# Optimization experiments

Measured on AMD Instinct MI355X. Metric: run time of the kernel, lower is better.

## Reference

```python
import jax, jax.numpy as jnp
import numpy as np


def setup_inputs() -> dict:
    key = jax.random.key(0)
    k1, k2, k3 = jax.random.split(key, 3)
    num, c_in, c_out, nx, ny, din, dout = 128, 3, 8, 31, 31, 4, 6
    x = jax.random.normal(k1, (num, c_in, din, nx + 1, ny + 1), dtype=jnp.float32)
    tensors = jax.random.normal(k2, (c_in, c_out, nx, ny, din, din, din, din, dout), dtype=jnp.float32)
    bias = jax.random.normal(k3, (c_out, nx, ny, dout), dtype=jnp.float32) * 1e-8
    return {"x": x, "tensors": tensors, "bias": bias}


def reference(x, tensors, bias):
    # x: [num, c_in, din, sx, sy]; tensors: [c_in, c_out, nx, ny, din,din,din,din, dout]
    num, c_in, din, sx, sy = x.shape
    X, Y = sx - 1, sy - 1  # == nx, ny
    c_out, dout = tensors.shape[1], tensors.shape[-1]
    # four 2x2-patch corners, each [num, c_in, din, X, Y]
    a = x[:, :, :, :-1, :-1]
    b = x[:, :, :, 1:, :-1]
    c = x[:, :, :, :-1, 1:]
    d = x[:, :, :, 1:, 1:]
    # outer product of the four corner vectors -> rank-4 local feature [num, c_in, din^4, X, Y]
    ab = jnp.einsum('ncixy,ncjxy->ncijxy', a, b)
    cd = jnp.einsum('nckxy,nclxy->ncklxy', c, d)
    patch = jnp.einsum('ncijxy,ncklxy->ncijklxy', ab, cd)
    patch = patch.reshape(num, c_in, din ** 4, X, Y)
    # per-position weight: [c_in, c_out, X, Y, din^4, dout]
    w = tensors.reshape(c_in, c_out, X, Y, din ** 4, dout)
    out = jnp.einsum('ncmxy,cpxymo->npoxy', patch, w)  # [num, c_out, dout, X, Y]
    out = out + bias.transpose(0, 3, 1, 2)[None]  # bias -> [1, c_out, dout, X, Y]
    return out
```

## Files before the change

### kernel.cpp

```cpp
#include <hip/hip_runtime.h>
#include <hip/hip_bf16.h>


typedef __attribute__((ext_vector_type(8))) short short8;
typedef __attribute__((ext_vector_type(4))) float floatx4;

#define WS_ELEMS (961u * 6144u)
#define SW_COLS 136

static __device__ __forceinline__ unsigned pkbf(float lo, float hi) {
  __hip_bfloat162 h = __float22bfloat162_rn(make_float2(lo, hi));
  union { __hip_bfloat162 h; unsigned u; } v;
  v.h = h;
  return v.u;
}

template <bool TO_WS>
__global__ __launch_bounds__(256, 4)
void ttn_conv_mfma(const float* __restrict__ x,
                   const float* __restrict__ tensors,
                   const float* __restrict__ bias,
                   float* __restrict__ dst) {
  __shared__ __align__(16) unsigned short sW[2][48 * SW_COLS];

  const int site = blockIdx.x;
  const int xx = site / 31, yy = site - xx * 31;
  const int t = threadIdx.x;
  const int lane = t & 63, wave = t >> 6;
  const int row = lane & 15, quad = lane >> 4;

  const int p_st = t >> 5, q_st = t & 31;

  floatx4 acc[2][3];
#pragma unroll
  for (int i0 = 0; i0 < 2; ++i0)
#pragma unroll
    for (int j0 = 0; j0 < 3; ++j0)
      acc[i0][j0] = (floatx4){0.f, 0.f, 0.f, 0.f};

  float a4[2][4], b2[2][2], cd8[2][8];
  float2 rAC[2][4], rBD[2][4];
  float4 wv[6];

  auto loadPair = [&](int s) {
    const int c = s >> 1;
    const float* base = tensors + ((size_t)((c * 8 + p_st) * 961 + site)) * 1536;
#pragma unroll
    for (int h = 0; h < 2; ++h) {
      const float* src = base + (size_t)((2 * (s & 1) + h) * 64 + 2 * q_st) * 6;
      wv[h * 3 + 0] = *(const float4*)src;
      wv[h * 3 + 1] = *(const float4*)(src + 4);
      wv[h * 3 + 2] = *(const float4*)(src + 8);
    }
  };
  auto storePair = [&](int buf) {
#pragma unroll
    for (int h = 0; h < 2; ++h) {
      const float4 w0 = wv[h * 3], w1 = wv[h * 3 + 1], w2 = wv[h * 3 + 2];
      const float vv[12] = {w0.x, w0.y, w0.z, w0.w, w1.x, w1.y,
                            w1.z, w1.w, w2.x, w2.y, w2.z, w2.w};
#pragma unroll
      for (int o = 0; o < 6; ++o)
        *(unsigned*)&sW[buf][(p_st * 6 + o) * SW_COLS + h * 64 + 2 * q_st] =
            pkbf(vv[o], vv[o + 6]);
    }
  };
  auto loadRaw = [&](int c) {
#pragma unroll
    for (int mt = 0; mt < 2; ++mt) {
      const int n = wave * 32 + mt * 16 + row;
      const float* xb = x + ((size_t)n * 3 + c) * 4096 + xx * 32 + yy;
#pragma unroll
      for (int i = 0; i < 4; ++i) {
        rAC[mt][i] = *(const float2*)(xb + i * 1024);
        rBD[mt][i] = *(const float2*)(xb + i * 1024 + 32);
      }
    }
  };
  auto cvtFactors = [&]() {
    const int qh = quad >> 1, ql = quad & 1;
#pragma unroll
    for (int mt = 0; mt < 2; ++mt) {
#pragma unroll
      for (int i = 0; i < 4; ++i) a4[mt][i] = rAC[mt][i].x;
      b2[mt][0] = qh ? rBD[mt][1].x : rBD[mt][0].x;
      b2[mt][1] = qh ? rBD[mt][3].x : rBD[mt][2].x;
      const float cq0 = ql ? rAC[mt][2].y : rAC[mt][0].y;
      const float cq1 = ql ? rAC[mt][3].y : rAC[mt][1].y;
#pragma unroll
      for (int j = 0; j < 8; ++j)
        cd8[mt][j] = (j < 4 ? cq0 : cq1) * rBD[mt][j & 3].y;
    }
  };

  loadPair(0);
  loadRaw(0);
  cvtFactors();
  storePair(0);
  loadPair(1);
  __syncthreads();

#pragma unroll
  for (int s = 0; s < 6; ++s) {
    const int bp = s & 1;
    if (s <= 4) storePair(1 - bp);
    if (s <= 3) loadPair(s + 2);
    if (s == 1) loadRaw(1);
    if (s == 3) loadRaw(2);
    if (s == 2 || s == 4) cvtFactors();

#pragma unroll
    for (int ks = 0; ks < 4; ++ks) {
      const int mb = 2 * (s & 1) + (ks >> 1);
      short8 bfr[3];
#pragma unroll
      for (int nt = 0; nt < 3; ++nt)
        bfr[nt] = *(const short8*)&sW[bp][(nt * 16 + row) * SW_COLS + ks * 32 + quad * 8];
#pragma unroll
      for (int mt = 0; mt < 2; ++mt) {
        const float ab = a4[mt][mb] * b2[mt][ks & 1];
        union { unsigned u[4]; short8 s8; } af;
#pragma unroll
        for (int jj = 0; jj < 4; ++jj)
          af.u[jj] = pkbf(ab * cd8[mt][2 * jj], ab * cd8[mt][2 * jj + 1]);
#pragma unroll
        for (int nt = 0; nt < 3; ++nt)
          acc[mt][nt] = __builtin_amdgcn_mfma_f32_16x16x32_bf16(
              af.s8, bfr[nt], acc[mt][nt], 0, 0, 0);
      }
    }
    if (s < 5) __syncthreads();
  }

  if (TO_WS) {
#pragma unroll
    for (int mt = 0; mt < 2; ++mt)
#pragma unroll
      for (int r = 0; r < 4; ++r) {
        const int n = wave * 32 + mt * 16 + quad * 4 + r;
#pragma unroll
        for (int nt = 0; nt < 3; ++nt) {
          const int po = nt * 16 + row;
          dst[(size_t)site * 6144 + n * 48 + po] = acc[mt][nt][r];
        }
      }
  } else {
#pragma unroll
    for (int mt = 0; mt < 2; ++mt)
#pragma unroll
      for (int r = 0; r < 4; ++r) {
        const int n = wave * 32 + mt * 16 + quad * 4 + r;
#pragma unroll
        for (int nt = 0; nt < 3; ++nt) {
          const int po = nt * 16 + row;
          const int p = po / 6, o = po - p * 6;
          dst[(size_t)(n * 48 + po) * 961 + site] =
              acc[mt][nt][r] + bias[(p * 961 + site) * 6 + o];
        }
      }
  }
}

__global__ __launch_bounds__(256, 8)
void ttn_transpose_bias(const float* __restrict__ ws,
                        const float* __restrict__ bias,
                        float* __restrict__ out) {
  __shared__ float tile[32][33];
  const int f0 = blockIdx.x * 32;
  const int s0 = blockIdx.y * 32;
  const int tx = threadIdx.x;
  const int ty = threadIdx.y;

#pragma unroll
  for (int rr = 0; rr < 4; ++rr) {
    const int srow = ty + rr * 8;
    const int site = s0 + srow;
    if (site < 961)
      tile[srow][tx] = ws[(size_t)site * 6144 + f0 + tx];
  }
  __syncthreads();

#pragma unroll
  for (int rr = 0; rr < 4; ++rr) {
    const int fy = ty + rr * 8;
    const int f = f0 + fy;
    const int site = s0 + tx;
    if (site < 961) {
      const int po = f % 48;
      const int p = po / 6, o = po - p * 6;
      out[(size_t)f * 961 + site] = tile[tx][fy] + bias[(p * 961 + site) * 6 + o];
    }
  }
}

extern "C" void kernel_launch(void* const* d_in, const int* in_sizes, int n_in,
                              void* d_out, int out_size, void* d_ws, size_t ws_size,
                              hipStream_t stream) {
  const float* x       = (const float*)d_in[0];
  const float* tensors = (const float*)d_in[1];
  const float* bias    = (const float*)d_in[2];
  float* out           = (float*)d_out;

  const size_t need = (size_t)WS_ELEMS * sizeof(float);
  if (d_ws != nullptr && ws_size >= need) {
    float* ws = (float*)d_ws;
    hipLaunchKernelGGL((ttn_conv_mfma<true>), dim3(961), dim3(256), 0, stream,
                       x, tensors, bias, ws);
    hipLaunchKernelGGL(ttn_transpose_bias, dim3(192, 31), dim3(32, 8), 0, stream,
                       ws, bias, out);
  } else {
    hipLaunchKernelGGL((ttn_conv_mfma<false>), dim3(961), dim3(256), 0, stream,
                       x, tensors, bias, out);
  }
}
```

Measured before the change: 245.4 us.

## Pre-convert weights to bf16 MFMA layout and feed GEMM from registers

Adds a separate pass that converts the fp32 per-site weights into bf16 in a layout matching the MFMA B-fragment. The GEMM kernel then loads those fragments straight from global memory into double-buffered registers. This removes the shared-memory staging, the in-loop bf16 packing and the block barriers from the main kernel. The cost is an extra kernel launch, roughly double the total weight traffic (read fp32, write bf16, read bf16 again) and a larger workspace requirement. The old fused path is kept as a fallback when the workspace is too small.

```diff
diff --git a/kernel.cpp b/kernel.cpp
--- a/kernel.cpp
+++ b/kernel.cpp
@@ -6,7 +6,8 @@
 typedef __attribute__((ext_vector_type(4))) float floatx4;
 
 #define WS_ELEMS (961u * 6144u)
-#define SW_COLS 136
+#define WP_OFFSET (32u * 1024u * 1024u)
+#define WP_BYTES ((size_t)23064u * 3072u)
 
 static __device__ __forceinline__ unsigned pkbf(float lo, float hi) {
   __hip_bfloat162 h = __float22bfloat162_rn(make_float2(lo, hi));
@@ -15,21 +16,39 @@
   return v.u;
 }
 
-template <bool TO_WS>
-__global__ __launch_bounds__(256, 4)
-void ttn_conv_mfma(const float* __restrict__ x,
-                   const float* __restrict__ tensors,
-                   const float* __restrict__ bias,
-                   float* __restrict__ dst) {
-  __shared__ __align__(16) unsigned short sW[2][48 * SW_COLS];
-
+__global__ __launch_bounds__(256)
+void ttn_wprep(const float* __restrict__ tensors, unsigned* __restrict__ wp) {
+  const int idx = blockIdx.x * 256 + threadIdx.x;
+  const int cps = idx >> 7, q = idx & 127;
+  const float* src = tensors + (size_t)cps * 1536 + q * 12;
+  const float4 v0 = *(const float4*)src;
+  const float4 v1 = *(const float4*)(src + 4);
+  const float4 v2 = *(const float4*)(src + 8);
+  const float vv[12] = {v0.x, v0.y, v0.z, v0.w, v1.x, v1.y,
+                        v1.z, v1.w, v2.x, v2.y, v2.z, v2.w};
+  unsigned* dst = wp + (size_t)cps * 768 + q;
+#pragma unroll
+  for (int o = 0; o < 6; ++o)
+    dst[o * 128] = pkbf(vv[o], vv[o + 6]);
+}
+
+__global__ __launch_bounds__(256, 3)
+void ttn_gemm(const float* __restrict__ x,
+              const unsigned short* __restrict__ wp,
+              float* __restrict__ ws) {
   const int site = blockIdx.x;
   const int xx = site / 31, yy = site - xx * 31;
-  const int t = threadIdx.x;
-  const int lane = t & 63, wave = t >> 6;
+  const int t = threadIdx.x, lane = t & 63, wave = t >> 6;
   const int row = lane & 15, quad = lane >> 4;
 
-  const int p_st = t >> 5, q_st = t & 31;
+  int baseo[3];
+#pragma unroll
+  for (int nt = 0; nt < 3; ++nt) {
+    const int po = nt * 16 + row;
+    const int p = po / 6, o = po - p * 6;
+    baseo[nt] = (p * 961 + site) * 1536 + o * 256 + quad * 8;
+  }
+  const size_t cstride = (size_t)8 * 961 * 1536;
 
   floatx4 acc[2][3];
 #pragma unroll
@@ -39,86 +58,54 @@
       acc[i0][j0] = (floatx4){0.f, 0.f, 0.f, 0.f};
 
   float a4[2][4], b2[2][2], cd8[2][8];
-  float2 rAC[2][4], rBD[2][4];
-  float4 wv[6];
-
-  auto loadPair = [&](int s) {
-    const int c = s >> 1;
-    const float* base = tensors + ((size_t)((c * 8 + p_st) * 961 + site)) * 1536;
-#pragma unroll
-    for (int h = 0; h < 2; ++h) {
-      const float* src = base + (size_t)((2 * (s & 1) + h) * 64 + 2 * q_st) * 6;
-      wv[h * 3 + 0] = *(const float4*)src;
-      wv[h * 3 + 1] = *(const float4*)(src + 4);
-      wv[h * 3 + 2] = *(const float4*)(src + 8);
-    }
-  };
-  auto storePair = [&](int buf) {
-#pragma unroll
-    for (int h = 0; h < 2; ++h) {
-      const float4 w0 = wv[h * 3], w1 = wv[h * 3 + 1], w2 = wv[h * 3 + 2];
-      const float vv[12] = {w0.x, w0.y, w0.z, w0.w, w1.x, w1.y,
-                            w1.z, w1.w, w2.x, w2.y, w2.z, w2.w};
-#pragma unroll
-      for (int o = 0; o < 6; ++o)
-        *(unsigned*)&sW[buf][(p_st * 6 + o) * SW_COLS + h * 64 + 2 * q_st] =
-            pkbf(vv[o], vv[o + 6]);
-    }
-  };
-  auto loadRaw = [&](int c) {
+  short8 wbuf[2][6];
+
+  auto loadChunk = [&](int ch, int buf) {
+    const unsigned short* base = wp + (size_t)(ch >> 2) * cstride + (ch & 3) * 64;
+#pragma unroll
+    for (int nt = 0; nt < 3; ++nt)
+#pragma unroll
+      for (int ks = 0; ks < 2; ++ks)
+        wbuf[buf][nt * 2 + ks] = *(const short8*)(base + baseo[nt] + ks * 32);
+  };
+  auto loadFactors = [&](int c) {
+    const int qh = quad >> 1, ql = quad & 1;
 #pragma unroll
     for (int mt = 0; mt < 2; ++mt) {
       const int n = wave * 32 + mt * 16 + row;
       const float* xb = x + ((size_t)n * 3 + c) * 4096 + xx * 32 + yy;
+      float2 rAC[4], rBD[4];
 #pragma unroll
       for (int i = 0; i < 4; ++i) {
-        rAC[mt][i] = *(const float2*)(xb + i * 1024);
-        rBD[mt][i] = *(const float2*)(xb + i * 1024 + 32);
-      }
-    }
-  };
-  auto cvtFactors = [&]() {
-    const int qh = quad >> 1, ql = quad & 1;
-#pragma unroll
-    for (int mt = 0; mt < 2; ++mt) {
-#pragma unroll
-      for (int i = 0; i < 4; ++i) a4[mt][i] = rAC[mt][i].x;
-      b2[mt][0] = qh ? rBD[mt][1].x : rBD[mt][0].x;
-      b2[mt][1] = qh ? rBD[mt][3].x : rBD[mt][2].x;
-      const float cq0 = ql ? rAC[mt][2].y : rAC[mt][0].y;
-      const float cq1 = ql ? rAC[mt][3].y : rAC[mt][1].y;
+        rAC[i] = *(const float2*)(xb + i * 1024);
+        rBD[i] = *(const float2*)(xb + i * 1024 + 32);
+      }
+#pragma unroll
+      for (int i = 0; i < 4; ++i) a4[mt][i] = rAC[i].x;
+      b2[mt][0] = qh ? rBD[1].x : rBD[0].x;
+      b2[mt][1] = qh ? rBD[3].x : rBD[2].x;
+      const float cq0 = ql ? rAC[2].y : rAC[0].y;
+      const float cq1 = ql ? rAC[3].y : rAC[1].y;
 #pragma unroll
       for (int j = 0; j < 8; ++j)
-        cd8[mt][j] = (j < 4 ? cq0 : cq1) * rBD[mt][j & 3].y;
-    }
-  };
-
-  loadPair(0);
-  loadRaw(0);
-  cvtFactors();
-  storePair(0);
-  loadPair(1);
-  __syncthreads();
-
-#pragma unroll
-  for (int s = 0; s < 6; ++s) {
-    const int bp = s & 1;
-    if (s <= 4) storePair(1 - bp);
-    if (s <= 3) loadPair(s + 2);
-    if (s == 1) loadRaw(1);
-    if (s == 3) loadRaw(2);
-    if (s == 2 || s == 4) cvtFactors();
-
-#pragma unroll
-    for (int ks = 0; ks < 4; ++ks) {
-      const int mb = 2 * (s & 1) + (ks >> 1);
-      short8 bfr[3];
-#pragma unroll
-      for (int nt = 0; nt < 3; ++nt)
-        bfr[nt] = *(const short8*)&sW[bp][(nt * 16 + row) * SW_COLS + ks * 32 + quad * 8];
+        cd8[mt][j] = (j < 4 ? cq0 : cq1) * rBD[j & 3].y;
+    }
+  };
+
+  loadFactors(0);
+  loadChunk(0, 0);
+
+#pragma unroll
+  for (int ch = 0; ch < 12; ++ch) {
+    const int cur = ch & 1;
+    if (ch == 4 || ch == 8) loadFactors(ch >> 2);
+    if (ch < 11) loadChunk(ch + 1, cur ^ 1);
+    const int mb = ch & 3;
+#pragma unroll
+    for (int ks = 0; ks < 2; ++ks)
 #pragma unroll
       for (int mt = 0; mt < 2; ++mt) {
-        const float ab = a4[mt][mb] * b2[mt][ks & 1];
+        const float ab = a4[mt][mb] * b2[mt][ks];
         union { unsigned u[4]; short8 s8; } af;
 #pragma unroll
         for (int jj = 0; jj < 4; ++jj)
@@ -126,39 +113,19 @@
 #pragma unroll
         for (int nt = 0; nt < 3; ++nt)
           acc[mt][nt] = __builtin_amdgcn_mfma_f32_16x16x32_bf16(
-              af.s8, bfr[nt], acc[mt][nt], 0, 0, 0);
-      }
-    }
-    if (s < 5) __syncthreads();
-  }
-
-  if (TO_WS) {
-#pragma unroll
-    for (int mt = 0; mt < 2; ++mt)
-#pragma unroll
-      for (int r = 0; r < 4; ++r) {
-        const int n = wave * 32 + mt * 16 + quad * 4 + r;
-#pragma unroll
-        for (int nt = 0; nt < 3; ++nt) {
-          const int po = nt * 16 + row;
-          dst[(size_t)site * 6144 + n * 48 + po] = acc[mt][nt][r];
-        }
-      }
-  } else {
-#pragma unroll
-    for (int mt = 0; mt < 2; ++mt)
-#pragma unroll
-      for (int r = 0; r < 4; ++r) {
-        const int n = wave * 32 + mt * 16 + quad * 4 + r;
-#pragma unroll
-        for (int nt = 0; nt < 3; ++nt) {
-          const int po = nt * 16 + row;
-          const int p = po / 6, o = po - p * 6;
-          dst[(size_t)(n * 48 + po) * 961 + site] =
-              acc[mt][nt][r] + bias[(p * 961 + site) * 6 + o];
-        }
-      }
-  }
+              af.s8, wbuf[cur][nt * 2 + ks], acc[mt][nt], 0, 0, 0);
+      }
+  }
+
+#pragma unroll
+  for (int mt = 0; mt < 2; ++mt)
+#pragma unroll
+    for (int r = 0; r < 4; ++r) {
+      const int n = wave * 32 + mt * 16 + quad * 4 + r;
+#pragma unroll
+      for (int nt = 0; nt < 3; ++nt)
+        ws[(size_t)site * 6144 + n * 48 + nt * 16 + row] = acc[mt][nt][r];
+    }
 }
 
 __global__ __launch_bounds__(256, 8)
@@ -168,8 +135,7 @@
   __shared__ float tile[32][33];
   const int f0 = blockIdx.x * 32;
   const int s0 = blockIdx.y * 32;
-  const int tx = threadIdx.x;
-  const int ty = threadIdx.y;
+  const int tx = threadIdx.x, ty = threadIdx.y;
 
 #pragma unroll
   for (int rr = 0; rr < 4; ++rr) {
@@ -193,6 +159,126 @@
   }
 }
 
+#define SW_COLS 136
+__global__ __launch_bounds__(256, 4)
+void ttn_conv_direct(const float* __restrict__ x,
+                     const float* __restrict__ tensors,
+                     const float* __restrict__ bias,
+                     float* __restrict__ dst) {
+  __shared__ __align__(16) unsigned short sW[2][48 * SW_COLS];
+  const int site = blockIdx.x;
+  const int xx = site / 31, yy = site - xx * 31;
+  const int t = threadIdx.x, lane = t & 63, wave = t >> 6;
+  const int row = lane & 15, quad = lane >> 4;
+  const int p_st = t >> 5, q_st = t & 31;
+
+  floatx4 acc[2][3];
+#pragma unroll
+  for (int i0 = 0; i0 < 2; ++i0)
+#pragma unroll
+    for (int j0 = 0; j0 < 3; ++j0)
+      acc[i0][j0] = (floatx4){0.f, 0.f, 0.f, 0.f};
+  float a4[2][4], b2[2][2], cd8[2][8];
+  float2 rAC[2][4], rBD[2][4];
+  float4 wv[6];
+
+  auto loadPair = [&](int s) {
+    const float* base = tensors + ((size_t)(((s >> 1) * 8 + p_st) * 961 + site)) * 1536;
+#pragma unroll
+    for (int h = 0; h < 2; ++h) {
+      const float* src = base + (size_t)((2 * (s & 1) + h) * 64 + 2 * q_st) * 6;
+      wv[h * 3 + 0] = *(const float4*)src;
+      wv[h * 3 + 1] = *(const float4*)(src + 4);
+      wv[h * 3 + 2] = *(const float4*)(src + 8);
+    }
+  };
+  auto storePair = [&](int buf) {
+#pragma unroll
+    for (int h = 0; h < 2; ++h) {
+      const float4 w0 = wv[h * 3], w1 = wv[h * 3 + 1], w2 = wv[h * 3 + 2];
+      const float vv[12] = {w0.x, w0.y, w0.z, w0.w, w1.x, w1.y,
+                            w1.z, w1.w, w2.x, w2.y, w2.z, w2.w};
+#pragma unroll
+      for (int o = 0; o < 6; ++o)
+        *(unsigned*)&sW[buf][(p_st * 6 + o) * SW_COLS + h * 64 + 2 * q_st] =
+            pkbf(vv[o], vv[o + 6]);
+    }
+  };
+  auto loadRaw = [&](int c) {
+#pragma unroll
+    for (int mt = 0; mt < 2; ++mt) {
+      const int n = wave * 32 + mt * 16 + row;
+      const float* xb = x + ((size_t)n * 3 + c) * 4096 + xx * 32 + yy;
+#pragma unroll
+      for (int i = 0; i < 4; ++i) {
+        rAC[mt][i] = *(const float2*)(xb + i * 1024);
+        rBD[mt][i] = *(const float2*)(xb + i * 1024 + 32);
+      }
+    }
+  };
+  auto cvtFactors = [&]() {
+    const int qh = quad >> 1, ql = quad & 1;
+#pragma unroll
+    for (int mt = 0; mt < 2; ++mt) {
+#pragma unroll
+      for (int i = 0; i < 4; ++i) a4[mt][i] = rAC[mt][i].x;
+      b2[mt][0] = qh ? rBD[mt][1].x : rBD[mt][0].x;
+      b2[mt][1] = qh ? rBD[mt][3].x : rBD[mt][2].x;
+      const float cq0 = ql ? rAC[mt][2].y : rAC[mt][0].y;
+      const float cq1 = ql ? rAC[mt][3].y : rAC[mt][1].y;
+#pragma unroll
+      for (int j = 0; j < 8; ++j)
+        cd8[mt][j] = (j < 4 ? cq0 : cq1) * rBD[mt][j & 3].y;
+    }
+  };
+
+  loadPair(0); loadRaw(0); cvtFactors(); storePair(0); loadPair(1);
+  __syncthreads();
+#pragma unroll
+  for (int s = 0; s < 6; ++s) {
+    const int bp = s & 1;
+    if (s <= 4) storePair(1 - bp);
+    if (s <= 3) loadPair(s + 2);
+    if (s == 1) loadRaw(1);
+    if (s == 3) loadRaw(2);
+    if (s == 2 || s == 4) cvtFactors();
+#pragma unroll
+    for (int ks = 0; ks < 4; ++ks) {
+      const int mb = 2 * (s & 1) + (ks >> 1);
+      short8 bfr[3];
+#pragma unroll
+      for (int nt = 0; nt < 3; ++nt)
+        bfr[nt] = *(const short8*)&sW[bp][(nt * 16 + row) * SW_COLS + ks * 32 + quad * 8];
+#pragma unroll
+      for (int mt = 0; mt < 2; ++mt) {
+        const float ab = a4[mt][mb] * b2[mt][ks & 1];
+        union { unsigned u[4]; short8 s8; } af;
+#pragma unroll
+        for (int jj = 0; jj < 4; ++jj)
+          af.u[jj] = pkbf(ab * cd8[mt][2 * jj], ab * cd8[mt][2 * jj + 1]);
+#pragma unroll
+        for (int nt = 0; nt < 3; ++nt)
+          acc[mt][nt] = __builtin_amdgcn_mfma_f32_16x16x32_bf16(
+              af.s8, bfr[nt], acc[mt][nt], 0, 0, 0);
+      }
+    }
+    if (s < 5) __syncthreads();
+  }
+#pragma unroll
+  for (int mt = 0; mt < 2; ++mt)
+#pragma unroll
+    for (int r = 0; r < 4; ++r) {
+      const int n = wave * 32 + mt * 16 + quad * 4 + r;
+#pragma unroll
+      for (int nt = 0; nt < 3; ++nt) {
+        const int po = nt * 16 + row;
+        const int p = po / 6, o = po - p * 6;
+        dst[(size_t)(n * 48 + po) * 961 + site] =
+            acc[mt][nt][r] + bias[(p * 961 + site) * 6 + o];
+      }
+    }
+}
+
 extern "C" void kernel_launch(void* const* d_in, const int* in_sizes, int n_in,
                               void* d_out, int out_size, void* d_ws, size_t ws_size,
                               hipStream_t stream) {
@@ -201,15 +287,17 @@
   const float* bias    = (const float*)d_in[2];
   float* out           = (float*)d_out;
 
-  const size_t need = (size_t)WS_ELEMS * sizeof(float);
+  const size_t need = (size_t)WP_OFFSET + WP_BYTES;
   if (d_ws != nullptr && ws_size >= need) {
     float* ws = (float*)d_ws;
-    hipLaunchKernelGGL((ttn_conv_mfma<true>), dim3(961), dim3(256), 0, stream,
-                       x, tensors, bias, ws);
+    unsigned* wp = (unsigned*)((char*)d_ws + WP_OFFSET);
+    hipLaunchKernelGGL(ttn_wprep, dim3(11532), dim3(256), 0, stream, tensors, wp);
+    hipLaunchKernelGGL(ttn_gemm, dim3(961), dim3(256), 0, stream,
+                       x, (const unsigned short*)wp, ws);
     hipLaunchKernelGGL(ttn_transpose_bias, dim3(192, 31), dim3(32, 8), 0, stream,
                        ws, bias, out);
   } else {
-    hipLaunchKernelGGL((ttn_conv_mfma<false>), dim3(961), dim3(256), 0, stream,
+    hipLaunchKernelGGL(ttn_conv_direct, dim3(961), dim3(256), 0, stream,
                        x, tensors, bias, out);
   }
 }
```

Result: slower. 292.2 us (+19.1%).
